# Optimization experiments

Hardware: AMD Instinct MI355X
Metric: run time of the kernel (lower is better)

## Reference

```python
import jax, jax.numpy as jnp
import numpy as np
import math

B, S, H, D = 4, 4096, 16, 64

def setup_inputs() -> dict:
    key = jax.random.key(0)
    k1, k2 = jax.random.split(key)
    qkv = jax.random.normal(k1, (B, S, 3, H, D), dtype=jnp.float32)
    key_padding_mask = jax.random.randint(k2, (B, S), 0, 2).astype(jnp.bool_)
    return {"qkv": qkv, "key_padding_mask": key_padding_mask}

def reference(qkv, key_padding_mask):
    # Faithful to FlashAtten_pytorch2_func: qkv (nnz,3,h,d) is unsqueezed to
    # (1,nnz,h,d) before SDPA, so SDPA treats nnz as batch and the HEADS dim
    # as the sequence dim -> each token attends over its own heads (h x h).
    # The unpad/pad round-trip is therefore equivalent to per-token attention
    # followed by zeroing padded positions (index_put into zeros buffer).
    q = qkv[:, :, 0]  # (B,S,H,D)
    k = qkv[:, :, 1]
    v = qkv[:, :, 2]
    scale = 1.0 / math.sqrt(D)  # softmax_scale=None -> 1/sqrt(headdim)
    scores = jnp.einsum('bshd,bsgd->bshg', q, k) * scale  # (B,S,H,H)
    attn = jax.nn.softmax(scores, axis=-1)
    out = jnp.einsum('bshg,bsgd->bshd', attn, v)  # (B,S,H,D)
    # padded tokens were never scattered back -> remain zero
    out = out * key_padding_mask[:, :, None, None].astype(out.dtype)
    return out
```

## Files before the change

### kernel.cpp

```cpp
#include <hip/hip_runtime.h>
#include <hip/hip_bf16.h>


typedef __attribute__((ext_vector_type(8))) short short8;
typedef __attribute__((ext_vector_type(4))) float floatx4;

static __device__ __forceinline__ short f2bf(float x) {
    union { __hip_bfloat16 b; short s; } u; u.b = __float2bfloat16(x);
    return u.s;
}
static __device__ __forceinline__ float bf2f(short s) {
    union { float f; unsigned int u; } u;
    u.u = ((unsigned int)(unsigned short)s) << 16;
    return u.f;
}
static __device__ __forceinline__ void split8(floatx4 a, floatx4 b,
                                              short8& hi, short8& lo) {
    float v[8] = {a[0], a[1], a[2], a[3], b[0], b[1], b[2], b[3]};
    #pragma unroll
    for (int j = 0; j < 8; ++j) {
        short h = f2bf(v[j]);
        hi[j] = h;
        lo[j] = f2bf(v[j] - bf2f(h));
    }
}

__global__ void detect_mask_fmt(const unsigned char* __restrict__ mb, int npos,
                                int* __restrict__ flag)
{
    __shared__ int found1, found2;
    if (threadIdx.x == 0) { found1 = 0; found2 = 0; }
    __syncthreads();
    int l1 = 0;
    for (int i = threadIdx.x; i < npos; i += blockDim.x)
        if ((i & 3) != 0 && mb[i] != 0) l1 = 1;
    if (l1) atomicOr(&found1, 1);
    __syncthreads();
    if (found1 == 0) {
        int l2 = 0;
        for (int i = threadIdx.x; i < npos / 2; i += blockDim.x)
            if (mb[8 * i + 4] != 0) l2 = 1;
        if (l2) atomicOr(&found2, 1);
        __syncthreads();
    } else {
        __syncthreads();
    }
    if (threadIdx.x == 0) *flag = found1 ? 0 : (found2 ? 1 : 2);
}

__global__ __launch_bounds__(256) void fa_heads_kernel(
    const float* __restrict__ qkv,
    const unsigned char* __restrict__ maskraw,
    const int* __restrict__ fmt,
    float* __restrict__ out,
    int npos)
{
    const int wid = (blockIdx.x << 2) + (threadIdx.x >> 6);
    if (wid >= npos) return;
    const int lane = threadIdx.x & 63;
    const int t  = lane & 15;
    const int qa = lane >> 4;

    const float* base = qkv + (size_t)wid * 3072;
    const float* Qp = base;
    const float* Kp = base + 1024;
    const float* Vp = base + 2048;

    const int fo = t * 64 + qa * 8;
    short8 khi0, klo0, khi1, klo1, qhi0, qlo0, qhi1, qlo1;
    split8(*(const floatx4*)(Kp + fo),      *(const floatx4*)(Kp + fo + 4),  khi0, klo0);
    split8(*(const floatx4*)(Kp + fo + 32), *(const floatx4*)(Kp + fo + 36), khi1, klo1);
    split8(*(const floatx4*)(Qp + fo),      *(const floatx4*)(Qp + fo + 4),  qhi0, qlo0);
    split8(*(const floatx4*)(Qp + fo + 32), *(const floatx4*)(Qp + fo + 36), qhi1, qlo1);

    floatx4 sc = {0.f, 0.f, 0.f, 0.f};
    sc = __builtin_amdgcn_mfma_f32_16x16x32_bf16(khi0, qhi0, sc, 0, 0, 0);
    sc = __builtin_amdgcn_mfma_f32_16x16x32_bf16(khi1, qhi1, sc, 0, 0, 0);
    sc = __builtin_amdgcn_mfma_f32_16x16x32_bf16(khi0, qlo0, sc, 0, 0, 0);
    sc = __builtin_amdgcn_mfma_f32_16x16x32_bf16(khi1, qlo1, sc, 0, 0, 0);
    sc = __builtin_amdgcn_mfma_f32_16x16x32_bf16(klo0, qhi0, sc, 0, 0, 0);
    sc = __builtin_amdgcn_mfma_f32_16x16x32_bf16(klo1, qhi1, sc, 0, 0, 0);

    float s0 = sc[0] * 0.125f, s1 = sc[1] * 0.125f;
    float s2 = sc[2] * 0.125f, s3 = sc[3] * 0.125f;
    float m = fmaxf(fmaxf(s0, s1), fmaxf(s2, s3));
    m = fmaxf(m, __shfl_xor(m, 16));
    m = fmaxf(m, __shfl_xor(m, 32));
    float e0 = __expf(s0 - m), e1 = __expf(s1 - m);
    float e2 = __expf(s2 - m), e3 = __expf(s3 - m);
    float l = e0 + e1 + e2 + e3;
    l += __shfl_xor(l, 16);
    l += __shfl_xor(l, 32);
    float rl = 1.0f / l;
    float p0 = e0 * rl, p1 = e1 * rl, p2 = e2 * rl, p3 = e3 * rl;

    int slo = (t + 32 * qa) & 63;
    int shi = (slo + 16) & 63;
    float av[8];
    av[0] = __shfl(p0, slo); av[1] = __shfl(p1, slo);
    av[2] = __shfl(p2, slo); av[3] = __shfl(p3, slo);
    av[4] = __shfl(p0, shi); av[5] = __shfl(p1, shi);
    av[6] = __shfl(p2, shi); av[7] = __shfl(p3, shi);
    const bool live = (qa < 2);
    short8 aph, apl;
    #pragma unroll
    for (int j = 0; j < 8; ++j) {
        short h = live ? f2bf(av[j]) : (short)0;
        aph[j] = h;
        apl[j] = live ? f2bf(av[j] - bf2f(h)) : (short)0;
    }

    floatx4 o[4];
    #pragma unroll
    for (int c = 0; c < 4; ++c) {
        short8 bvh, bvl;
        #pragma unroll
        for (int j = 0; j < 8; ++j) {
            int g = (8 * qa + j) & 15;
            float v = Vp[g * 64 + c * 16 + t];
            short h = f2bf(v);
            bvh[j] = h;
            bvl[j] = f2bf(v - bf2f(h));
        }
        floatx4 z = {0.f, 0.f, 0.f, 0.f};
        z = __builtin_amdgcn_mfma_f32_16x16x32_bf16(aph, bvh, z, 0, 0, 0);
        z = __builtin_amdgcn_mfma_f32_16x16x32_bf16(aph, bvl, z, 0, 0, 0);
        z = __builtin_amdgcn_mfma_f32_16x16x32_bf16(apl, bvh, z, 0, 0, 0);
        o[c] = z;
    }

    const int f = *fmt;
    int mi;
    if (f == 0)       mi = (int)maskraw[wid];
    else if (f == 1)  mi = ((const int*)maskraw)[wid];
    else              mi = (int)(((const long long*)maskraw)[wid] != 0);
    const float mv = (mi != 0) ? 1.0f : 0.0f;

    float* op = out + (size_t)wid * 1024;
    #pragma unroll
    for (int c = 0; c < 4; ++c) {
        #pragma unroll
        for (int r = 0; r < 4; ++r) {
            op[(4 * qa + r) * 64 + c * 16 + t] = o[c][r] * mv;
        }
    }
}

extern "C" void kernel_launch(void* const* d_in, const int* in_sizes, int n_in,
                              void* d_out, int out_size, void* d_ws, size_t ws_size,
                              hipStream_t stream) {
    const float* qkv = (const float*)d_in[0];
    const unsigned char* maskraw = (const unsigned char*)d_in[1];
    float* out = (float*)d_out;
    int* fmt = (int*)d_ws;
    const int npos = in_sizes[1];

    detect_mask_fmt<<<1, 256, 0, stream>>>(maskraw, npos, fmt);

    const int blocks = (npos + 3) / 4;
    fa_heads_kernel<<<blocks, 256, 0, stream>>>(qkv, maskraw, fmt, out, npos);
}
```

Measured before the change: 330.9 us.

## Hoist V and mask loads, split MFMA accumulator chains, widen mask detection

The mask detection kernel now runs with 1024 threads and scans the mask in 16-byte vector loads instead of byte by byte. The main kernel issues the mask and all V loads up front, so memory latency overlaps with the QK^T MFMAs. The dependent MFMA chains are split into two independent accumulators that are summed afterwards, shortening the dependency chains. Hoisting all V loads raises register pressure, which may lower occupancy.

```diff
diff --git a/kernel.cpp b/kernel.cpp
--- a/kernel.cpp
+++ b/kernel.cpp
@@ -25,26 +25,32 @@
     }
 }
 
-__global__ void detect_mask_fmt(const unsigned char* __restrict__ mb, int npos,
-                                int* __restrict__ flag)
+__global__ __launch_bounds__(1024) void detect_mask_fmt(
+    const unsigned char* __restrict__ mb, int npos, int* __restrict__ flag)
 {
     __shared__ int found1, found2;
     if (threadIdx.x == 0) { found1 = 0; found2 = 0; }
     __syncthreads();
+
     int l1 = 0;
-    for (int i = threadIdx.x; i < npos; i += blockDim.x)
+    const int nvec = npos >> 4;
+    const uint4* v = (const uint4*)mb;
+    for (int i = threadIdx.x; i < nvec; i += blockDim.x) {
+        uint4 w = v[i];
+        if ((w.x | w.y | w.z | w.w) & 0xFFFFFF00u) l1 = 1;
+    }
+    for (int i = (nvec << 4) + threadIdx.x; i < npos; i += blockDim.x)
         if ((i & 3) != 0 && mb[i] != 0) l1 = 1;
     if (l1) atomicOr(&found1, 1);
     __syncthreads();
+
     if (found1 == 0) {
         int l2 = 0;
         for (int i = threadIdx.x; i < npos / 2; i += blockDim.x)
             if (mb[8 * i + 4] != 0) l2 = 1;
         if (l2) atomicOr(&found2, 1);
-        __syncthreads();
-    } else {
-        __syncthreads();
     }
+    __syncthreads();
     if (threadIdx.x == 0) *flag = found1 ? 0 : (found2 ? 1 : 2);
 }
 
@@ -66,6 +72,13 @@
     const float* Kp = base + 1024;
     const float* Vp = base + 2048;
 
+    const int f = *fmt;
+    int mi;
+    if (f == 0)       mi = (int)maskraw[wid];
+    else if (f == 1)  mi = ((const int*)maskraw)[wid];
+    else              mi = (int)(((const long long*)maskraw)[wid] != 0);
+    const float mv = (mi != 0) ? 1.0f : 0.0f;
+
     const int fo = t * 64 + qa * 8;
     short8 khi0, klo0, khi1, klo1, qhi0, qlo0, qhi1, qlo1;
     split8(*(const floatx4*)(Kp + fo),      *(const floatx4*)(Kp + fo + 4),  khi0, klo0);
@@ -73,13 +86,30 @@
     split8(*(const floatx4*)(Qp + fo),      *(const floatx4*)(Qp + fo + 4),  qhi0, qlo0);
     split8(*(const floatx4*)(Qp + fo + 32), *(const floatx4*)(Qp + fo + 36), qhi1, qlo1);
 
-    floatx4 sc = {0.f, 0.f, 0.f, 0.f};
-    sc = __builtin_amdgcn_mfma_f32_16x16x32_bf16(khi0, qhi0, sc, 0, 0, 0);
-    sc = __builtin_amdgcn_mfma_f32_16x16x32_bf16(khi1, qhi1, sc, 0, 0, 0);
-    sc = __builtin_amdgcn_mfma_f32_16x16x32_bf16(khi0, qlo0, sc, 0, 0, 0);
-    sc = __builtin_amdgcn_mfma_f32_16x16x32_bf16(khi1, qlo1, sc, 0, 0, 0);
-    sc = __builtin_amdgcn_mfma_f32_16x16x32_bf16(klo0, qhi0, sc, 0, 0, 0);
-    sc = __builtin_amdgcn_mfma_f32_16x16x32_bf16(klo1, qhi1, sc, 0, 0, 0);
+    short8 bvh[4], bvl[4];
+    #pragma unroll
+    for (int c = 0; c < 4; ++c) {
+        #pragma unroll
+        for (int j = 0; j < 8; ++j) {
+            int g = (8 * qa + j) & 15;
+            float vv = Vp[g * 64 + c * 16 + t];
+            short h = f2bf(vv);
+            bvh[c][j] = h;
+            bvl[c][j] = f2bf(vv - bf2f(h));
+        }
+    }
+
+    floatx4 sa = {0.f, 0.f, 0.f, 0.f};
+    floatx4 sb = {0.f, 0.f, 0.f, 0.f};
+    sa = __builtin_amdgcn_mfma_f32_16x16x32_bf16(khi0, qhi0, sa, 0, 0, 0);
+    sb = __builtin_amdgcn_mfma_f32_16x16x32_bf16(khi1, qhi1, sb, 0, 0, 0);
+    sa = __builtin_amdgcn_mfma_f32_16x16x32_bf16(khi0, qlo0, sa, 0, 0, 0);
+    sb = __builtin_amdgcn_mfma_f32_16x16x32_bf16(khi1, qlo1, sb, 0, 0, 0);
+    sa = __builtin_amdgcn_mfma_f32_16x16x32_bf16(klo0, qhi0, sa, 0, 0, 0);
+    sb = __builtin_amdgcn_mfma_f32_16x16x32_bf16(klo1, qhi1, sb, 0, 0, 0);
+    floatx4 sc;
+    sc[0] = sa[0] + sb[0]; sc[1] = sa[1] + sb[1];
+    sc[2] = sa[2] + sb[2]; sc[3] = sa[3] + sb[3];
 
     float s0 = sc[0] * 0.125f, s1 = sc[1] * 0.125f;
     float s2 = sc[2] * 0.125f, s3 = sc[3] * 0.125f;
@@ -113,28 +143,14 @@
     floatx4 o[4];
     #pragma unroll
     for (int c = 0; c < 4; ++c) {
-        short8 bvh, bvl;
-        #pragma unroll
-        for (int j = 0; j < 8; ++j) {
-            int g = (8 * qa + j) & 15;
-            float v = Vp[g * 64 + c * 16 + t];
-            short h = f2bf(v);
-            bvh[j] = h;
-            bvl[j] = f2bf(v - bf2f(h));
-        }
         floatx4 z = {0.f, 0.f, 0.f, 0.f};
-        z = __builtin_amdgcn_mfma_f32_16x16x32_bf16(aph, bvh, z, 0, 0, 0);
-        z = __builtin_amdgcn_mfma_f32_16x16x32_bf16(aph, bvl, z, 0, 0, 0);
-        z = __builtin_amdgcn_mfma_f32_16x16x32_bf16(apl, bvh, z, 0, 0, 0);
-        o[c] = z;
+        floatx4 w = {0.f, 0.f, 0.f, 0.f};
+        z = __builtin_amdgcn_mfma_f32_16x16x32_bf16(aph, bvh[c], z, 0, 0, 0);
+        w = __builtin_amdgcn_mfma_f32_16x16x32_bf16(aph, bvl[c], w, 0, 0, 0);
+        w = __builtin_amdgcn_mfma_f32_16x16x32_bf16(apl, bvh[c], w, 0, 0, 0);
+        o[c][0] = z[0] + w[0]; o[c][1] = z[1] + w[1];
+        o[c][2] = z[2] + w[2]; o[c][3] = z[3] + w[3];
     }
-
-    const int f = *fmt;
-    int mi;
-    if (f == 0)       mi = (int)maskraw[wid];
-    else if (f == 1)  mi = ((const int*)maskraw)[wid];
-    else              mi = (int)(((const long long*)maskraw)[wid] != 0);
-    const float mv = (mi != 0) ? 1.0f : 0.0f;
 
     float* op = out + (size_t)wid * 1024;
     #pragma unroll
@@ -155,7 +171,7 @@
     int* fmt = (int*)d_ws;
     const int npos = in_sizes[1];
 
-    detect_mask_fmt<<<1, 256, 0, stream>>>(maskraw, npos, fmt);
+    detect_mask_fmt<<<1, 1024, 0, stream>>>(maskraw, npos, fmt);
 
     const int blocks = (npos + 3) / 4;
     fa_heads_kernel<<<blocks, 256, 0, stream>>>(qkv, maskraw, fmt, out, npos);
```

New measurement: 295.7 us. -10.6%, faster.
